# Kernel optimization log

Hardware: AMD Instinct MI355X
Metric: run time of the kernel (lower is better)

The kernel has to match this reference:

```python
import jax, jax.numpy as jnp
import numpy as np

D_MODEL = 1024
D_FF = 4096
BATCH = 4
SEQ = 2048
DECAY = 0.9
THRESH = 0.5


def setup_inputs() -> dict:
    key = jax.random.key(0)
    k1, k2, k3, k4 = jax.random.split(key, 4)
    spikes = jax.random.normal(k1, (BATCH, SEQ, D_MODEL), dtype=jnp.float32)
    # xavier-ish init scales matching gains 0.5/0.5/0.3 in the torch module
    s1 = 0.5 * np.sqrt(2.0 / (D_MODEL + D_FF))
    s2 = 0.5 * np.sqrt(2.0 / (D_MODEL + D_FF))
    sr = 0.3 * np.sqrt(2.0 / (D_MODEL + D_FF))
    W1 = jax.random.normal(k2, (D_FF, D_MODEL), dtype=jnp.float32) * s1
    W2 = jax.random.normal(k3, (D_MODEL, D_FF), dtype=jnp.float32) * s2
    Wr = jax.random.normal(k4, (D_FF, D_MODEL), dtype=jnp.float32) * sr
    return {"spikes": spikes, "W1": W1, "W2": W2, "Wr": Wr}


def reference(spikes, W1, W2, Wr):
    # spikes: [B, T, D]; W1, Wr: [F, D]; W2: [D, F]
    B, T, D = spikes.shape
    F = W1.shape[0]
    d = jnp.float32(DECAY)
    one_minus_d = jnp.float32(1.0 - DECAY)
    # Hoist time-independent projections out of the recurrence (same math as
    # the per-timestep nn.Linear calls in the torch loop).
    r_all = jax.nn.sigmoid(jnp.einsum('btd,fd->btf', spikes, Wr))  # [B,T,F]
    h_all = jnp.einsum('btd,fd->btf', spikes, W1)                   # [B,T,F]

    def step(carry, xs):
        act, rec = carry              # [B,F] each, init zeros (fresh buffers)
        r_t, h_t = xs                 # [B,F]
        rec = d * rec + one_minus_d * r_t                 # mixed receptance
        mixed = d * act + one_minus_d * h_t               # temporal state mix
        spike = (mixed > THRESH).astype(h_t.dtype)        # eval-mode spikes
        gated = spike * r_t
        # torch detaches current_activation each step
        return (jax.lax.stop_gradient(mixed), rec), gated

    init = (jnp.zeros((B, F), spikes.dtype), jnp.zeros((B, F), spikes.dtype))
    _, gated = jax.lax.scan(step,
                            init,
                            (jnp.swapaxes(r_all, 0, 1), jnp.swapaxes(h_all, 0, 1)))
    # gated: [T, B, F] -> output [B, T, D]
    out = jnp.einsum('tbf,df->btd', gated, W2)
    return out
```

## Files before the change

### kernel.cpp

```cpp
#include <hip/hip_runtime.h>
#include <math.h>

#define B_    4
#define T_    2048
#define D_    1024
#define F_    4096
#define R_    (B_*T_)
#define SEG_  64
#define L_    (T_/SEG_)
#define DECAYF 0.9f
#define OMDF   0.1f
#define FLAG_THRESH 0.45f

typedef __attribute__((ext_vector_type(4)))  int   i32x4;
typedef __attribute__((ext_vector_type(8)))  int   i32x8;
typedef __attribute__((ext_vector_type(16))) float f32x16;

__device__ __forceinline__ int pk_fp8x4(float x, float y, float z, float w) {
    int p = 0;
    p = __builtin_amdgcn_cvt_pk_fp8_f32(x, y, p, false);
    p = __builtin_amdgcn_cvt_pk_fp8_f32(z, w, p, true);
    return p;
}

__device__ __forceinline__ size_t pk_off(int row, int d) {
    return ((size_t)((row >> 5) * 16 + (d >> 6)) * 2048)
         + ((d >> 4) & 1) * 1024
         + ((row & 31) + ((d >> 5) & 1) * 32) * 16
         + (d & 15);
}

#define KA_W1_BLOCKS  4096
#define KA_SEG_BLOCKS 256
#define KA_FLAG_BLOCKS 32

__global__ __launch_bounds__(256)
void kA_prologue(const float* __restrict__ spikes,
                 const float* __restrict__ W1,
                 unsigned char* __restrict__ w_f8,
                 float* __restrict__ seg_sum,
                 unsigned int* __restrict__ flags) {
    const int bid = blockIdx.x;
    const int tid = threadIdx.x;
    if (bid < KA_W1_BLOCKS) {
        int i = bid * 256 + tid;
        float4 v = ((const float4*)W1)[i];
        int f  = i >> 8;
        int d0 = (i & 255) * 4;
        *(int*)(w_f8 + pk_off(f, d0)) = pk_fp8x4(8.f*v.x, 8.f*v.y, 8.f*v.z, 8.f*v.w);
    } else if (bid < KA_W1_BLOCKS + KA_SEG_BLOCKS) {
        int t = (bid - KA_W1_BLOCKS) * 256 + tid;
        int dg = t & (D_ / 4 - 1);
        int s = (t >> 8) & (SEG_ - 1);
        int b = t >> 14;
        const float4* sp4 = (const float4*)spikes;
        const int base = (b * T_ + s * L_) * (D_ / 4) + dg;
        float4 e = {0.f, 0.f, 0.f, 0.f};
#pragma unroll 8
        for (int k = 0; k < L_; ++k) {
            float4 x = sp4[base + k * (D_ / 4)];
            e.x = DECAYF * e.x + OMDF * x.x;
            e.y = DECAYF * e.y + OMDF * x.y;
            e.z = DECAYF * e.z + OMDF * x.z;
            e.w = DECAYF * e.w + OMDF * x.w;
        }
        ((float4*)seg_sum)[(b * SEG_ + s) * (D_ / 4) + dg] = e;
    } else {
        int i = (bid - KA_W1_BLOCKS - KA_SEG_BLOCKS) * 256 + tid;
        if (i < R_) flags[i] = 0u;
    }
}

__global__ __launch_bounds__(256)
void kB_seg_scan(const float* __restrict__ seg_sum,
                 float* __restrict__ start_state) {
    int g = blockIdx.x * 256 + threadIdx.x;
    int s = g & 63;
    int c = g >> 6;
    int d = c & (D_ - 1);
    int b = c >> 10;
    int idx = (b * SEG_ + s) * D_ + d;
    float v = seg_sum[idx];
    float wp = 0.0343368382f;
#pragma unroll
    for (int off = 1; off < SEG_; off <<= 1) {
        float u = __shfl_up(v, off, 64);
        if (s >= off) v += wp * u;
        wp *= wp;
    }
    float pv = __shfl_up(v, 1, 64);
    start_state[idx] = (s == 0) ? 0.f : pv;
}

__global__ __launch_bounds__(256)
void kC_ema_fp8(const float* __restrict__ spikes,
                const float* __restrict__ start_state,
                unsigned char* __restrict__ a_f8) {
    int t = blockIdx.x * 256 + threadIdx.x;
    int dg = t & (D_ / 4 - 1);
    int s = (t >> 8) & (SEG_ - 1);
    int b = t >> 14;
    const float4* sp4 = (const float4*)spikes;
    const int base = (b * T_ + s * L_) * (D_ / 4) + dg;
    const int d0 = dg * 4;
    unsigned char* dst = a_f8 + pk_off(b * T_ + s * L_, d0);
    float4 e = ((const float4*)start_state)[(b * SEG_ + s) * (D_ / 4) + dg];
#pragma unroll 8
    for (int k = 0; k < L_; ++k) {
        float4 x = sp4[base + k * (D_ / 4)];
        e.x = DECAYF * e.x + OMDF * x.x;
        e.y = DECAYF * e.y + OMDF * x.y;
        e.z = DECAYF * e.z + OMDF * x.z;
        e.w = DECAYF * e.w + OMDF * x.w;
        *(int*)(dst + k * 16) = pk_fp8x4(8.f*e.x, 8.f*e.y, 8.f*e.z, 8.f*e.w);
    }
}

__global__ __launch_bounds__(256)
void k2_mfma_flags(const unsigned char* __restrict__ Ap,
                   const unsigned char* __restrict__ Bp,
                   unsigned int* __restrict__ flags) {
    const int tid = threadIdx.x;
    const int w = tid >> 6;
    const int lane = tid & 63;
    const int m0 = blockIdx.y * 128;
    const int n0 = blockIdx.x * 128;
    const int wm = w >> 1, wn = w & 1;
    const int kg = lane >> 5;

    const unsigned char* a0 = Ap + ((size_t)((m0 >> 5) + wm * 2 + 0) * 16) * 2048 + lane * 16;
    const unsigned char* a1 = Ap + ((size_t)((m0 >> 5) + wm * 2 + 1) * 16) * 2048 + lane * 16;
    const unsigned char* b0 = Bp + ((size_t)((n0 >> 5) + wn * 2 + 0) * 16) * 2048 + lane * 16;
    const unsigned char* b1 = Bp + ((size_t)((n0 >> 5) + wn * 2 + 1) * 16) * 2048 + lane * 16;

    f32x16 acc[2][2] = {};

#define LDFRAG(p, C)                                                        \
    ({ i32x4 lo_ = *(const i32x4*)((p) + (size_t)(C) * 2048);               \
       i32x4 hi_ = *(const i32x4*)((p) + (size_t)(C) * 2048 + 1024);        \
       (i32x8){lo_.x, lo_.y, lo_.z, lo_.w, hi_.x, hi_.y, hi_.z, hi_.w}; })

#define MFMA4(AF0, AF1, BF0, BF1)                                           \
    {                                                                       \
        acc[0][0] = __builtin_amdgcn_mfma_scale_f32_32x32x64_f8f6f4(        \
            AF0, BF0, acc[0][0], 0, 0, 0, 124, 0, 124);                     \
        acc[0][1] = __builtin_amdgcn_mfma_scale_f32_32x32x64_f8f6f4(        \
            AF0, BF1, acc[0][1], 0, 0, 0, 124, 0, 124);                     \
        acc[1][0] = __builtin_amdgcn_mfma_scale_f32_32x32x64_f8f6f4(        \
            AF1, BF0, acc[1][0], 0, 0, 0, 124, 0, 124);                     \
        acc[1][1] = __builtin_amdgcn_mfma_scale_f32_32x32x64_f8f6f4(        \
            AF1, BF1, acc[1][1], 0, 0, 0, 124, 0, 124);                     \
    }

    i32x8 A0a = LDFRAG(a0, 0), A1a = LDFRAG(a1, 0);
    i32x8 B0a = LDFRAG(b0, 0), B1a = LDFRAG(b1, 0);
#pragma unroll
    for (int C = 0; C < 16; C += 2) {
        i32x8 A0b = LDFRAG(a0, C + 1), A1b = LDFRAG(a1, C + 1);
        i32x8 B0b = LDFRAG(b0, C + 1), B1b = LDFRAG(b1, C + 1);
        MFMA4(A0a, A1a, B0a, B1a);
        const int C2 = (C + 2) & 15;
        A0a = LDFRAG(a0, C2); A1a = LDFRAG(a1, C2);
        B0a = LDFRAG(b0, C2); B1a = LDFRAG(b1, C2);
        MFMA4(A0b, A1b, B0b, B1b);
    }
#undef LDFRAG
#undef MFMA4

#pragma unroll
    for (int i = 0; i < 2; ++i) {
#pragma unroll
        for (int reg = 0; reg < 16; ++reg) {
            float mx = fmaxf(acc[i][0][reg], acc[i][1][reg]);
            if (mx > FLAG_THRESH) {
                const int rr = (reg & 3) + 8 * (reg >> 2) + 4 * kg;
                atomicOr(&flags[m0 + wm * 64 + i * 32 + rr], 1u);
            }
        }
    }
}

__global__ __launch_bounds__(256)
void k4_output(const float* __restrict__ spikes,
               const float* __restrict__ start_state,
               const float* __restrict__ W1,
               const float* __restrict__ Wr,
               const float* __restrict__ W2,
               const unsigned int* __restrict__ flags,
               float* __restrict__ out) {
    const int row = blockIdx.x;
    const int tid = threadIdx.x;
    float4 o = {0.f, 0.f, 0.f, 0.f};

    if (flags[row] == 0u) {
        *(float4*)&out[(size_t)row * D_ + tid * 4] = o;
        return;
    }

    __shared__ float se[D_];
    __shared__ float sp[D_];
    __shared__ float red[256];
    __shared__ int nspk;
    __shared__ int spk_list[256];

    const int b = row / T_;
    const int t = row % T_;
    const int seg = t / L_;
    const int off = t % L_;
    const int segbase = (b * T_ + seg * L_) * D_;

    for (int i = tid; i < D_; i += 256) {
        float e = start_state[(b * SEG_ + seg) * D_ + i];
        for (int j = 0; j <= off; ++j)
            e = DECAYF * e + OMDF * spikes[segbase + j * D_ + i];
        se[i] = e;
        sp[i] = spikes[(size_t)row * D_ + i];
    }
    if (tid == 0) nspk = 0;
    __syncthreads();

    for (int f0 = 0; f0 < F_; f0 += 256) {
        int f = f0 + tid;
        float mix = 0.f;
        for (int k = 0; k < D_; ++k) mix += se[k] * W1[(size_t)f * D_ + k];
        if (mix > 0.5f) {
            int idx = atomicAdd(&nspk, 1);
            spk_list[idx] = f;
        }
        __syncthreads();
        int n = nspk;
        for (int i = 0; i < n; ++i) {
            int fs = spk_list[i];
            float part = 0.f;
#pragma unroll
            for (int k = 0; k < 4; ++k)
                part += sp[tid * 4 + k] * Wr[(size_t)fs * D_ + tid * 4 + k];
            red[tid] = part;
            __syncthreads();
            for (int sft = 128; sft > 0; sft >>= 1) {
                if (tid < sft) red[tid] += red[tid + sft];
                __syncthreads();
            }
            float r = 1.f / (1.f + expf(-red[0]));
            __syncthreads();
            o.x += r * W2[(size_t)(tid * 4 + 0) * F_ + fs];
            o.y += r * W2[(size_t)(tid * 4 + 1) * F_ + fs];
            o.z += r * W2[(size_t)(tid * 4 + 2) * F_ + fs];
            o.w += r * W2[(size_t)(tid * 4 + 3) * F_ + fs];
        }
        __syncthreads();
        if (tid == 0) nspk = 0;
        __syncthreads();
    }
    *(float4*)&out[(size_t)row * D_ + tid * 4] = o;
}

extern "C" void kernel_launch(void* const* d_in, const int* in_sizes, int n_in,
                              void* d_out, int out_size, void* d_ws, size_t ws_size,
                              hipStream_t stream) {
    const float* spikes = (const float*)d_in[0];
    const float* W1     = (const float*)d_in[1];
    const float* W2     = (const float*)d_in[2];
    const float* Wr     = (const float*)d_in[3];
    float* out = (float*)d_out;

    char* ws = (char*)d_ws;
    float* seg_sum      = (float*)ws;
    float* start_state  = seg_sum + (size_t)B_ * SEG_ * D_;
    unsigned int* flags = (unsigned int*)(start_state + (size_t)B_ * SEG_ * D_);
    unsigned char* a_f8 = (unsigned char*)(flags + R_);
    unsigned char* w_f8 = a_f8 + (size_t)R_ * D_;

    kA_prologue<<<KA_W1_BLOCKS + KA_SEG_BLOCKS + KA_FLAG_BLOCKS, 256, 0, stream>>>(
        spikes, W1, w_f8, seg_sum, flags);
    kB_seg_scan<<<(B_ * D_ * 64) / 256, 256, 0, stream>>>(seg_sum, start_state);
    kC_ema_fp8<<<(B_ * SEG_ * D_ / 4) / 256, 256, 0, stream>>>(spikes, start_state, a_f8);

    dim3 g2(F_ / 128, R_ / 128);
    k2_mfma_flags<<<g2, 256, 0, stream>>>(a_f8, w_f8, flags);

    k4_output<<<R_, 256, 0, stream>>>(spikes, start_state, W1, Wr, W2, flags, out);
}
```

Measured before the change: 186.7 us.

## Widen MFMA flag tile to 128x256 with 4-stage register prefetch and swizzled grid

```diff
diff --git a/kernel.cpp b/kernel.cpp
--- a/kernel.cpp
+++ b/kernel.cpp
@@ -11,6 +11,7 @@
 #define DECAYF 0.9f
 #define OMDF   0.1f
 #define FLAG_THRESH 0.45f
+
 
 typedef __attribute__((ext_vector_type(4)))  int   i32x4;
 typedef __attribute__((ext_vector_type(8)))  int   i32x8;
@@ -123,55 +124,78 @@
     const int tid = threadIdx.x;
     const int w = tid >> 6;
     const int lane = tid & 63;
-    const int m0 = blockIdx.y * 128;
-    const int n0 = blockIdx.x * 128;
+    const int orig = blockIdx.x;
+    const int swz  = (orig & 7) * 128 + (orig >> 3);
+    const int m0 = (swz >> 4) * 128;
+    const int n0 = (swz & 15) * 256;
     const int wm = w >> 1, wn = w & 1;
     const int kg = lane >> 5;
 
     const unsigned char* a0 = Ap + ((size_t)((m0 >> 5) + wm * 2 + 0) * 16) * 2048 + lane * 16;
     const unsigned char* a1 = Ap + ((size_t)((m0 >> 5) + wm * 2 + 1) * 16) * 2048 + lane * 16;
-    const unsigned char* b0 = Bp + ((size_t)((n0 >> 5) + wn * 2 + 0) * 16) * 2048 + lane * 16;
-    const unsigned char* b1 = Bp + ((size_t)((n0 >> 5) + wn * 2 + 1) * 16) * 2048 + lane * 16;
-
-    f32x16 acc[2][2] = {};
-
-#define LDFRAG(p, C)                                                        \
-    ({ i32x4 lo_ = *(const i32x4*)((p) + (size_t)(C) * 2048);               \
-       i32x4 hi_ = *(const i32x4*)((p) + (size_t)(C) * 2048 + 1024);        \
+    const unsigned char* b0 = Bp + ((size_t)((n0 >> 5) + wn * 4 + 0) * 16) * 2048 + lane * 16;
+    const unsigned char* b1 = Bp + ((size_t)((n0 >> 5) + wn * 4 + 1) * 16) * 2048 + lane * 16;
+    const unsigned char* b2 = Bp + ((size_t)((n0 >> 5) + wn * 4 + 2) * 16) * 2048 + lane * 16;
+    const unsigned char* b3 = Bp + ((size_t)((n0 >> 5) + wn * 4 + 3) * 16) * 2048 + lane * 16;
+
+    f32x16 acc[2][4] = {};
+
+#define LDF(p, OFF)                                                         \
+    ({ i32x4 lo_ = *(const i32x4*)((p) + (OFF));                            \
+       i32x4 hi_ = *(const i32x4*)((p) + (OFF) + 1024);                     \
        (i32x8){lo_.x, lo_.y, lo_.z, lo_.w, hi_.x, hi_.y, hi_.z, hi_.w}; })
 
-#define MFMA4(AF0, AF1, BF0, BF1)                                           \
-    {                                                                       \
-        acc[0][0] = __builtin_amdgcn_mfma_scale_f32_32x32x64_f8f6f4(        \
-            AF0, BF0, acc[0][0], 0, 0, 0, 124, 0, 124);                     \
-        acc[0][1] = __builtin_amdgcn_mfma_scale_f32_32x32x64_f8f6f4(        \
-            AF0, BF1, acc[0][1], 0, 0, 0, 124, 0, 124);                     \
-        acc[1][0] = __builtin_amdgcn_mfma_scale_f32_32x32x64_f8f6f4(        \
-            AF1, BF0, acc[1][0], 0, 0, 0, 124, 0, 124);                     \
-        acc[1][1] = __builtin_amdgcn_mfma_scale_f32_32x32x64_f8f6f4(        \
-            AF1, BF1, acc[1][1], 0, 0, 0, 124, 0, 124);                     \
-    }
-
-    i32x8 A0a = LDFRAG(a0, 0), A1a = LDFRAG(a1, 0);
-    i32x8 B0a = LDFRAG(b0, 0), B1a = LDFRAG(b1, 0);
-#pragma unroll
-    for (int C = 0; C < 16; C += 2) {
-        i32x8 A0b = LDFRAG(a0, C + 1), A1b = LDFRAG(a1, C + 1);
-        i32x8 B0b = LDFRAG(b0, C + 1), B1b = LDFRAG(b1, C + 1);
-        MFMA4(A0a, A1a, B0a, B1a);
-        const int C2 = (C + 2) & 15;
-        A0a = LDFRAG(a0, C2); A1a = LDFRAG(a1, C2);
-        B0a = LDFRAG(b0, C2); B1a = LDFRAG(b1, C2);
-        MFMA4(A0b, A1b, B0b, B1b);
-    }
-#undef LDFRAG
-#undef MFMA4
+#define MFMA1(i, j, AF, BF)                                                 \
+    acc[i][j] = __builtin_amdgcn_mfma_scale_f32_32x32x64_f8f6f4(            \
+        AF, BF, acc[i][j], 0, 0, 0, 124, 0, 124);
+
+#define MFMA8(S)                                                            \
+    MFMA1(0, 0, A0##S, B0##S) MFMA1(0, 1, A0##S, B1##S)                     \
+    MFMA1(0, 2, A0##S, B2##S) MFMA1(0, 3, A0##S, B3##S)                     \
+    MFMA1(1, 0, A1##S, B0##S) MFMA1(1, 1, A1##S, B1##S)                     \
+    MFMA1(1, 2, A1##S, B2##S) MFMA1(1, 3, A1##S, B3##S)
+
+#define LOADSTAGE(S, OFF)                                                   \
+    A0##S = LDF(a0, OFF); A1##S = LDF(a1, OFF);                             \
+    B0##S = LDF(b0, OFF); B1##S = LDF(b1, OFF);                             \
+    B2##S = LDF(b2, OFF); B3##S = LDF(b3, OFF);
+
+    i32x8 A0s0, A1s0, B0s0, B1s0, B2s0, B3s0;
+    i32x8 A0s1, A1s1, B0s1, B1s1, B2s1, B3s1;
+    i32x8 A0s2, A1s2, B0s2, B1s2, B2s2, B3s2;
+    i32x8 A0s3, A1s3, B0s3, B1s3, B2s3, B3s3;
+    LOADSTAGE(s0, 0)
+    LOADSTAGE(s1, 2048)
+    LOADSTAGE(s2, 4096)
+    LOADSTAGE(s3, 6144)
+
+#pragma unroll 1
+    for (int p = 0; p < 3; ++p) {
+        const size_t off = (size_t)(p + 1) * 8192;
+        MFMA8(s0)
+        LOADSTAGE(s0, off)
+        MFMA8(s1)
+        LOADSTAGE(s1, off + 2048)
+        MFMA8(s2)
+        LOADSTAGE(s2, off + 4096)
+        MFMA8(s3)
+        LOADSTAGE(s3, off + 6144)
+    }
+    MFMA8(s0)
+    MFMA8(s1)
+    MFMA8(s2)
+    MFMA8(s3)
+#undef LDF
+#undef MFMA1
+#undef MFMA8
+#undef LOADSTAGE
 
 #pragma unroll
     for (int i = 0; i < 2; ++i) {
 #pragma unroll
         for (int reg = 0; reg < 16; ++reg) {
-            float mx = fmaxf(acc[i][0][reg], acc[i][1][reg]);
+            float mx = fmaxf(fmaxf(acc[i][0][reg], acc[i][1][reg]),
+                             fmaxf(acc[i][2][reg], acc[i][3][reg]));
             if (mx > FLAG_THRESH) {
                 const int rr = (reg & 3) + 8 * (reg >> 2) + 4 * kg;
                 atomicOr(&flags[m0 + wm * 64 + i * 32 + rr], 1u);
@@ -276,8 +300,7 @@
     kB_seg_scan<<<(B_ * D_ * 64) / 256, 256, 0, stream>>>(seg_sum, start_state);
     kC_ema_fp8<<<(B_ * SEG_ * D_ / 4) / 256, 256, 0, stream>>>(spikes, start_state, a_f8);
 
-    dim3 g2(F_ / 128, R_ / 128);
-    k2_mfma_flags<<<g2, 256, 0, stream>>>(a_f8, w_f8, flags);
+    k2_mfma_flags<<<(R_ / 128) * (F_ / 256), 256, 0, stream>>>(a_f8, w_f8, flags);
 
     k4_output<<<R_, 256, 0, stream>>>(spikes, start_state, W1, Wr, W2, flags, out);
 }
```

Measured after the change: 174.3 us. 1.07x faster.
